# Kernel optimization log

Measured on AMD Instinct MI355X. Metric: run time of the kernel, lower is better.

The kernel has to match this reference:

```python
import jax, jax.numpy as jnp
import numpy as np

D_MODEL = 1024
N_HEADS = 16
D_K = D_MODEL // N_HEADS
NEG_INF = -1e30


def setup_inputs() -> dict:
    key = jax.random.key(0)
    ks = jax.random.split(key, 12)
    B, S = 4, 2048
    scale = 1.0 / np.sqrt(D_MODEL)
    inp = {
        "query": jax.random.normal(ks[0], (B, S, D_MODEL), jnp.float32),
        "key": jax.random.normal(ks[1], (B, S, D_MODEL), jnp.float32),
        "value": jax.random.normal(ks[2], (B, S, D_MODEL), jnp.float32),
        "mask": jax.random.randint(ks[3], (B, S, S), 0, 2, jnp.int32),
        "w_q": jax.random.normal(ks[4], (D_MODEL, D_MODEL), jnp.float32) * scale,
        "b_q": jnp.zeros((D_MODEL,), jnp.float32),
        "w_k": jax.random.normal(ks[5], (D_MODEL, D_MODEL), jnp.float32) * scale,
        "b_k": jnp.zeros((D_MODEL,), jnp.float32),
        "w_v": jax.random.normal(ks[6], (D_MODEL, D_MODEL), jnp.float32) * scale,
        "b_v": jnp.zeros((D_MODEL,), jnp.float32),
        "w_o": jax.random.normal(ks[7], (D_MODEL, D_MODEL), jnp.float32) * scale,
        "b_o": jnp.zeros((D_MODEL,), jnp.float32),
    }
    return inp


def reference(query, key, value, mask, w_q, b_q, w_k, b_k, w_v, b_v, w_o, b_o):
    B, Sq, _ = query.shape
    Sk = key.shape[1]
    # Linear projections (torch nn.Linear: x @ W.T + b), split into heads
    Q = (query @ w_q.T + b_q).reshape(B, Sq, N_HEADS, D_K).transpose(0, 2, 1, 3)
    K = (key @ w_k.T + b_k).reshape(B, Sk, N_HEADS, D_K).transpose(0, 2, 1, 3)
    V = (value @ w_v.T + b_v).reshape(B, Sk, N_HEADS, D_K).transpose(0, 2, 1, 3)
    # scores: (B, H, Sq, Sk)
    scores = jnp.einsum('bhqd,bhkd->bhqk', Q, K) / jnp.sqrt(jnp.float32(D_K))
    scores = jnp.where(mask[:, None, :, :] == 0, NEG_INF, scores)
    attn = jax.nn.softmax(scores, axis=-1)  # dropout p=0 -> identity (eval)
    context = jnp.einsum('bhqk,bhkd->bhqd', attn, V)
    context = context.transpose(0, 2, 1, 3).reshape(B, Sq, D_MODEL)
    return context @ w_o.T + b_o
```

## Files before the change

### kernel.cpp

```cpp
#include <hip/hip_runtime.h>
#include <hip/hip_bf16.h>
#include <stdint.h>

#define DM 1024
#define NHEADS 16
#define DK 64
#define BB 4
#define SS 2048

typedef unsigned short u16;
typedef __bf16 bf16x8 __attribute__((ext_vector_type(8)));
typedef __bf16 bf16x4 __attribute__((ext_vector_type(4)));
typedef float f32x4 __attribute__((ext_vector_type(4)));

#if __has_builtin(__builtin_amdgcn_exp2f)
#define EXP2(x) __builtin_amdgcn_exp2f(x)
#else
#define EXP2(x) exp2f(x)
#endif

static __device__ __forceinline__ u16 f2bf(float f) {
    union { float f; uint32_t u; } v; v.f = f;
    uint32_t r = v.u + 0x7fffu + ((v.u >> 16) & 1u);
    return (u16)(r >> 16);
}

static __device__ __forceinline__ f32x4 mfma16(bf16x8 a, bf16x8 b, f32x4 c) {
    return __builtin_amdgcn_mfma_f32_16x16x32_bf16(a, b, c, 0, 0, 0);
}

static __device__ __forceinline__ void gload16(const u16* g, u16* l) {
    __builtin_amdgcn_global_load_lds((const __attribute__((address_space(1))) void*)g,
                                     (__attribute__((address_space(3))) void*)l, 16, 0, 0);
}

#define PREP_W 4096
#define PREP_X 12288
#define PREP_M 2048
__global__ __launch_bounds__(256) void k_prep(const float* __restrict__ wq, const float* __restrict__ wk,
                                              const float* __restrict__ wv, const float* __restrict__ wo,
                                              u16* __restrict__ wout,
                                              const float* __restrict__ xq, const float* __restrict__ xk,
                                              const float* __restrict__ xv, u16* __restrict__ xout,
                                              const int* __restrict__ mask, uint32_t* __restrict__ bits) {
    const int bid = blockIdx.x, tid = threadIdx.x;
    if (bid < PREP_W) {
        int t = bid * 256 + tid;
        int which = t >> 18;
        int off = (t & 0x3FFFF) << 2;
        const float* src = (which == 0) ? wq : (which == 1) ? wk : (which == 2) ? wv : wo;
        float4 v = *(const float4*)(src + off);
        ushort4 o;
        o.x = f2bf(v.x); o.y = f2bf(v.y); o.z = f2bf(v.z); o.w = f2bf(v.w);
        *(ushort4*)(wout + ((size_t)which << 20) + off) = o;
    } else if (bid < PREP_W + PREP_X) {
        int lb = bid - PREP_W;
        int which = lb >> 12;
        const float* src = (which == 0) ? xq : (which == 1) ? xk : xv;
        size_t base = (((size_t)(lb & 4095)) * 256 + tid) * 8;
        float4 v0 = *(const float4*)(src + base);
        float4 v1 = *(const float4*)(src + base + 4);
        union { u16 s[8]; uint4 u; } p;
        p.s[0]=f2bf(v0.x); p.s[1]=f2bf(v0.y); p.s[2]=f2bf(v0.z); p.s[3]=f2bf(v0.w);
        p.s[4]=f2bf(v1.x); p.s[5]=f2bf(v1.y); p.s[6]=f2bf(v1.z); p.s[7]=f2bf(v1.w);
        *(uint4*)(xout + ((size_t)which << 23) + base) = p.u;
    } else {
        int lb = bid - PREP_W - PREP_X;
        int gid = lb * 256 + tid;
        int lane = gid & 63;
        int wv_ = gid >> 6;
        const int nw = (PREP_M * 256) >> 6;
        const long totalInts = (long)BB * SS * SS;
        for (long base = (long)wv_ * 64; base < totalInts; base += (long)nw * 64) {
            int m = mask[base + lane];
            unsigned long long bal = __ballot(m != 0);
            if (lane == 0)  bits[(base >> 5)]     = (uint32_t)bal;
            if (lane == 32) bits[(base >> 5) + 1] = (uint32_t)(bal >> 32);
        }
    }
}

template<int MODE>
__global__ __launch_bounds__(256) void k_proj(const u16* __restrict__ X, const u16* __restrict__ W,
                                              const float* __restrict__ bias, void* __restrict__ Yv,
                                              float alpha) {
    __shared__ u16 Ab[128 * 32];
    __shared__ u16 Bb[128 * 32];
    const int tid = threadIdx.x;
    const int lane = tid & 63, wv = tid >> 6;
    const int wr = wv >> 1, wc = wv & 1;
    const int lrow = lane & 15, lgrp = lane >> 4;
    const int m0 = (blockIdx.x >> 3) * 128;
    const int n0 = (blockIdx.x & 7) * 128;
    const int trow = tid >> 2;
    const int tk = (tid & 3) * 8;

    f32x4 acc[4][4] = {};

    for (int kk = 0; kk < DM; kk += 32) {
#pragma unroll
        for (int i = 0; i < 2; ++i) {
            gload16(X + (size_t)(m0 + i * 64 + trow) * DM + kk + tk, &Ab[(i * 256 + tid) * 8]);
            gload16(W + (size_t)(n0 + i * 64 + trow) * DM + kk + tk, &Bb[(i * 256 + tid) * 8]);
        }
        __syncthreads();
        bf16x8 af[4], bfr[4];
#pragma unroll
        for (int i = 0; i < 4; ++i)
            af[i] = *(const bf16x8*)&Ab[(wr * 64 + i * 16 + lrow) * 32 + lgrp * 8];
#pragma unroll
        for (int j = 0; j < 4; ++j)
            bfr[j] = *(const bf16x8*)&Bb[(wc * 64 + j * 16 + lrow) * 32 + lgrp * 8];
#pragma unroll
        for (int i = 0; i < 4; ++i)
#pragma unroll
            for (int j = 0; j < 4; ++j)
                acc[i][j] = mfma16(af[i], bfr[j], acc[i][j]);
        __syncthreads();
    }

#pragma unroll
    for (int j = 0; j < 4; ++j) {
        int n = n0 + wc * 64 + j * 16 + lrow;
        float bv = bias[n];
        int h = n >> 6, d = n & 63;
#pragma unroll
        for (int i = 0; i < 4; ++i) {
            int mbase = m0 + wr * 64 + i * 16 + (lgrp << 2);
            if (MODE == 0) {
                u16* Y = (u16*)Yv;
#pragma unroll
                for (int r = 0; r < 4; ++r) {
                    int m = mbase + r;
                    int b = m >> 11, s = m & 2047;
                    Y[(((size_t)(b * NHEADS + h) * SS) + s) * DK + d] = f2bf((acc[i][j][r] + bv) * alpha);
                }
            } else if (MODE == 1) {
                int b = mbase >> 11, s = mbase & 2047;
                ushort4 o;
                o.x = f2bf(acc[i][j][0] + bv);
                o.y = f2bf(acc[i][j][1] + bv);
                o.z = f2bf(acc[i][j][2] + bv);
                o.w = f2bf(acc[i][j][3] + bv);
                *(ushort4*)&((u16*)Yv)[(((size_t)(b * NHEADS + h) * DK) + d) * SS + s] = o;
            } else {
                float* Y = (float*)Yv;
#pragma unroll
                for (int r = 0; r < 4; ++r)
                    Y[(size_t)(mbase + r) * DM + n] = acc[i][j][r] + bv;
            }
        }
    }
}

#define NT (SS / 64)
__global__ __launch_bounds__(512, 4) void k_attn(const u16* __restrict__ Q, const u16* __restrict__ K,
                                                 const u16* __restrict__ VT, const uint32_t* __restrict__ mbits,
                                                 u16* __restrict__ ctx) {
    __shared__ u16 Kt[2][64 * 64];
    __shared__ u16 Vt[2][64 * 64];
    __shared__ u16 Pl[8][2][16][72];
    const int tid = threadIdx.x;
    const int lane = tid & 63, w = tid >> 6;
    const int lrow = lane & 15, lgrp = lane >> 4;
    const int bid = blockIdx.x;
    const int bh = bid & 63;
    const int qt = bid >> 6;
    const int b = bh >> 4, h = bh & 15;
    const int qbase = qt * 256 + w * 32;

    const u16* Qh = Q + (size_t)bh * SS * DK;
    const u16* Kh = K + (size_t)bh * SS * DK;
    const u16* Vh = VT + (size_t)bh * DK * SS;

    bf16x8 qf[2][2];
#pragma unroll
    for (int s = 0; s < 2; ++s) {
        const u16* p = Qh + (size_t)(qbase + 16 * s + lrow) * DK + lgrp * 8;
        qf[s][0] = *(const bf16x8*)(p);
        qf[s][1] = *(const bf16x8*)(p + 32);
    }

    const uint64_t* mrow[2];
#pragma unroll
    for (int s = 0; s < 2; ++s)
        mrow[s] = (const uint64_t*)mbits + ((size_t)(b * SS + qbase + 16 * s + lrow)) * (SS / 64);

    union { uint4 u; bf16x8 v; } onesu;
    onesu.u = make_uint4(0x3F803F80u, 0x3F803F80u, 0x3F803F80u, 0x3F803F80u);
    const bf16x8 ones = onesu.v;

    const int swzA = (lgrp * 8) ^ ((lrow & 7) * 8);
    const int swzB = (32 + lgrp * 8) ^ ((lrow & 7) * 8);

    const int srow = tid >> 3;
    const int ssrc = ((tid & 7) * 8) ^ ((srow & 7) * 8);

    f32x4 acc[2][4] = {};
    f32x4 asum[2] = {};

    gload16(Kh + (size_t)srow * DK + ssrc, &Kt[0][tid * 8]);
    gload16(Vh + (size_t)srow * SS + ssrc, &Vt[0][tid * 8]);
    __syncthreads();

    int cur = 0;
    for (int kt = 0; kt < NT; ++kt) {
        if (kt + 1 < NT) {
            gload16(Kh + (size_t)((kt + 1) * 64 + srow) * DK + ssrc, &Kt[cur ^ 1][tid * 8]);
            gload16(Vh + (size_t)srow * SS + (kt + 1) * 64 + ssrc, &Vt[cur ^ 1][tid * 8]);
        }
        uint64_t wm2[2];
#pragma unroll
        for (int s = 0; s < 2; ++s) wm2[s] = mrow[s][kt];

        const u16* Kc = Kt[cur];
        const u16* Vc = Vt[cur];
        bf16x8 pf[2][2];
#pragma unroll
        for (int s = 0; s < 2; ++s) {
            f32x4 st[4] = {};
#pragma unroll
            for (int t = 0; t < 4; ++t) {
                bf16x8 ka = *(const bf16x8*)&Kc[(16 * t + lrow) * 64 + swzA];
                bf16x8 kb = *(const bf16x8*)&Kc[(16 * t + lrow) * 64 + swzB];
                st[t] = mfma16(ka, qf[s][0], st[t]);
                st[t] = mfma16(kb, qf[s][1], st[t]);
            }
            const uint64_t wm = wm2[s];
#pragma unroll
            for (int t = 0; t < 4; ++t) {
                uint32_t wt = (uint32_t)(wm >> (16 * t + 4 * lgrp));
                bf16x4 pk;
#pragma unroll
                for (int r = 0; r < 4; ++r) {
                    float p = EXP2(st[t][r]);
                    p = ((wt >> r) & 1u) ? p : 0.0f;
                    pk[r] = (__bf16)p;
                }
                *(bf16x4*)&Pl[w][s][lrow][16 * t + 4 * lgrp] = pk;
            }
            pf[s][0] = *(const bf16x8*)&Pl[w][s][lrow][lgrp * 8];
            pf[s][1] = *(const bf16x8*)&Pl[w][s][lrow][32 + lgrp * 8];
            asum[s] = mfma16(pf[s][0], ones, asum[s]);
            asum[s] = mfma16(pf[s][1], ones, asum[s]);
        }
#pragma unroll
        for (int dt = 0; dt < 4; ++dt) {
            bf16x8 vf0 = *(const bf16x8*)&Vc[(16 * dt + lrow) * 64 + swzA];
            bf16x8 vf1 = *(const bf16x8*)&Vc[(16 * dt + lrow) * 64 + swzB];
#pragma unroll
            for (int s = 0; s < 2; ++s) {
                acc[s][dt] = mfma16(pf[s][0], vf0, acc[s][dt]);
                acc[s][dt] = mfma16(pf[s][1], vf1, acc[s][dt]);
            }
        }
        __syncthreads();
        cur ^= 1;
    }

#pragma unroll
    for (int s = 0; s < 2; ++s)
#pragma unroll
        for (int r = 0; r < 4; ++r) {
            float li = 1.0f / asum[s][r];
            int q = qbase + 16 * s + 4 * lgrp + r;
#pragma unroll
            for (int dt = 0; dt < 4; ++dt)
                ctx[((size_t)b * SS + q) * DM + h * 64 + dt * 16 + lrow] = f2bf(acc[s][dt][r] * li);
        }
}

extern "C" void kernel_launch(void* const* d_in, const int* in_sizes, int n_in,
                              void* d_out, int out_size, void* d_ws, size_t ws_size,
                              hipStream_t stream) {
    const float* query = (const float*)d_in[0];
    const float* key   = (const float*)d_in[1];
    const float* value = (const float*)d_in[2];
    const int*   mask  = (const int*)d_in[3];
    const float* w_q   = (const float*)d_in[4];
    const float* b_q   = (const float*)d_in[5];
    const float* w_k   = (const float*)d_in[6];
    const float* b_k   = (const float*)d_in[7];
    const float* w_v   = (const float*)d_in[8];
    const float* b_v   = (const float*)d_in[9];
    const float* w_o   = (const float*)d_in[10];
    const float* b_o   = (const float*)d_in[11];
    float* out = (float*)d_out;

    char* ws = (char*)d_ws;
    u16*      Wb = (u16*)(ws);
    uint32_t* mb = (uint32_t*)(ws + (8u  << 20));
    u16*      Xq = (u16*)(ws + (16u << 20));
    u16*      Xk = (u16*)(ws + (32u << 20));
    u16*      Xv = (u16*)(ws + (48u << 20));
    u16*      Qw = (u16*)(ws + (64u << 20));
    u16*      Kw = (u16*)(ws + (80u << 20));
    u16*      Vw = (u16*)(ws + (96u << 20));
    u16*      Cw = (u16*)(ws + (112u << 20));

    const float qscale = 0.125f * 1.4426950408889634f;

    k_prep<<<dim3(PREP_W + PREP_X + PREP_M), dim3(256), 0, stream>>>(
        w_q, w_k, w_v, w_o, Wb, query, key, value, Xq, mask, mb);
    k_proj<0><<<dim3(512), dim3(256), 0, stream>>>(Xq, Wb,              b_q, Qw, qscale);
    k_proj<0><<<dim3(512), dim3(256), 0, stream>>>(Xk, Wb + (1u << 20), b_k, Kw, 1.0f);
    k_proj<1><<<dim3(512), dim3(256), 0, stream>>>(Xv, Wb + (2u << 20), b_v, Vw, 1.0f);
    k_attn<<<dim3(512), dim3(512), 0, stream>>>(Qw, Kw, Vw, mb, Cw);
    k_proj<2><<<dim3(512), dim3(256), 0, stream>>>(Cw, Wb + (3u << 20), b_o, out, 1.0f);
}
```

Baseline: 278.7 us.

## Merge QKV projections into one launch and shrink attention P buffer

Combines the three Q/K/V projection GEMM launches into a single 1536-block kernel that selects inputs by block index, reducing launch overhead and tail effects. The attention kernel reuses one LDS P-staging slot per wave instead of two, halving that buffer, and raises the launch-bounds occupancy hint from 4 to 6. The tighter register budget may cause spills in the attention kernel.

```diff
diff --git a/kernel.cpp b/kernel.cpp
--- a/kernel.cpp
+++ b/kernel.cpp
@@ -80,10 +80,85 @@
     }
 }
 
-template<int MODE>
-__global__ __launch_bounds__(256) void k_proj(const u16* __restrict__ X, const u16* __restrict__ W,
-                                              const float* __restrict__ bias, void* __restrict__ Yv,
-                                              float alpha) {
+__global__ __launch_bounds__(256) void k_projqkv(const u16* __restrict__ Xq, const u16* __restrict__ Xk,
+                                                 const u16* __restrict__ Xv, const u16* __restrict__ Wb,
+                                                 const float* __restrict__ bq, const float* __restrict__ bk,
+                                                 const float* __restrict__ bv,
+                                                 u16* __restrict__ Qw, u16* __restrict__ Kw,
+                                                 u16* __restrict__ Vw, float qscale) {
+    __shared__ u16 Ab[128 * 32];
+    __shared__ u16 Bb[128 * 32];
+    const int sel = blockIdx.x >> 9;
+    const int tile = blockIdx.x & 511;
+    const u16* X = (sel == 0) ? Xq : (sel == 1) ? Xk : Xv;
+    const u16* W = Wb + ((size_t)sel << 20);
+    const float* bias = (sel == 0) ? bq : (sel == 1) ? bk : bv;
+    u16* Y = (sel == 0) ? Qw : (sel == 1) ? Kw : Vw;
+    const float alpha = (sel == 0) ? qscale : 1.0f;
+
+    const int tid = threadIdx.x;
+    const int lane = tid & 63, wv = tid >> 6;
+    const int wr = wv >> 1, wc = wv & 1;
+    const int lrow = lane & 15, lgrp = lane >> 4;
+    const int m0 = (tile >> 3) * 128;
+    const int n0 = (tile & 7) * 128;
+    const int trow = tid >> 2;
+    const int tk = (tid & 3) * 8;
+
+    f32x4 acc[4][4] = {};
+
+    for (int kk = 0; kk < DM; kk += 32) {
+#pragma unroll
+        for (int i = 0; i < 2; ++i) {
+            gload16(X + (size_t)(m0 + i * 64 + trow) * DM + kk + tk, &Ab[(i * 256 + tid) * 8]);
+            gload16(W + (size_t)(n0 + i * 64 + trow) * DM + kk + tk, &Bb[(i * 256 + tid) * 8]);
+        }
+        __syncthreads();
+        bf16x8 af[4], bfr[4];
+#pragma unroll
+        for (int i = 0; i < 4; ++i)
+            af[i] = *(const bf16x8*)&Ab[(wr * 64 + i * 16 + lrow) * 32 + lgrp * 8];
+#pragma unroll
+        for (int j = 0; j < 4; ++j)
+            bfr[j] = *(const bf16x8*)&Bb[(wc * 64 + j * 16 + lrow) * 32 + lgrp * 8];
+#pragma unroll
+        for (int i = 0; i < 4; ++i)
+#pragma unroll
+            for (int j = 0; j < 4; ++j)
+                acc[i][j] = mfma16(af[i], bfr[j], acc[i][j]);
+        __syncthreads();
+    }
+
+#pragma unroll
+    for (int j = 0; j < 4; ++j) {
+        int n = n0 + wc * 64 + j * 16 + lrow;
+        float bv_ = bias[n];
+        int h = n >> 6, d = n & 63;
+#pragma unroll
+        for (int i = 0; i < 4; ++i) {
+            int mbase = m0 + wr * 64 + i * 16 + (lgrp << 2);
+            if (sel != 2) {
+#pragma unroll
+                for (int r = 0; r < 4; ++r) {
+                    int m = mbase + r;
+                    int b = m >> 11, s = m & 2047;
+                    Y[(((size_t)(b * NHEADS + h) * SS) + s) * DK + d] = f2bf((acc[i][j][r] + bv_) * alpha);
+                }
+            } else {
+                int b = mbase >> 11, s = mbase & 2047;
+                ushort4 o;
+                o.x = f2bf(acc[i][j][0] + bv_);
+                o.y = f2bf(acc[i][j][1] + bv_);
+                o.z = f2bf(acc[i][j][2] + bv_);
+                o.w = f2bf(acc[i][j][3] + bv_);
+                *(ushort4*)&Y[(((size_t)(b * NHEADS + h) * DK) + d) * SS + s] = o;
+            }
+        }
+    }
+}
+
+__global__ __launch_bounds__(256) void k_oproj(const u16* __restrict__ X, const u16* __restrict__ W,
+                                               const float* __restrict__ bias, float* __restrict__ out) {
     __shared__ u16 Ab[128 * 32];
     __shared__ u16 Bb[128 * 32];
     const int tid = threadIdx.x;
@@ -123,43 +198,23 @@
     for (int j = 0; j < 4; ++j) {
         int n = n0 + wc * 64 + j * 16 + lrow;
         float bv = bias[n];
-        int h = n >> 6, d = n & 63;
 #pragma unroll
         for (int i = 0; i < 4; ++i) {
             int mbase = m0 + wr * 64 + i * 16 + (lgrp << 2);
-            if (MODE == 0) {
-                u16* Y = (u16*)Yv;
-#pragma unroll
-                for (int r = 0; r < 4; ++r) {
-                    int m = mbase + r;
-                    int b = m >> 11, s = m & 2047;
-                    Y[(((size_t)(b * NHEADS + h) * SS) + s) * DK + d] = f2bf((acc[i][j][r] + bv) * alpha);
-                }
-            } else if (MODE == 1) {
-                int b = mbase >> 11, s = mbase & 2047;
-                ushort4 o;
-                o.x = f2bf(acc[i][j][0] + bv);
-                o.y = f2bf(acc[i][j][1] + bv);
-                o.z = f2bf(acc[i][j][2] + bv);
-                o.w = f2bf(acc[i][j][3] + bv);
-                *(ushort4*)&((u16*)Yv)[(((size_t)(b * NHEADS + h) * DK) + d) * SS + s] = o;
-            } else {
-                float* Y = (float*)Yv;
-#pragma unroll
-                for (int r = 0; r < 4; ++r)
-                    Y[(size_t)(mbase + r) * DM + n] = acc[i][j][r] + bv;
-            }
+#pragma unroll
+            for (int r = 0; r < 4; ++r)
+                out[(size_t)(mbase + r) * DM + n] = acc[i][j][r] + bv;
         }
     }
 }
 
 #define NT (SS / 64)
-__global__ __launch_bounds__(512, 4) void k_attn(const u16* __restrict__ Q, const u16* __restrict__ K,
+__global__ __launch_bounds__(512, 6) void k_attn(const u16* __restrict__ Q, const u16* __restrict__ K,
                                                  const u16* __restrict__ VT, const uint32_t* __restrict__ mbits,
                                                  u16* __restrict__ ctx) {
     __shared__ u16 Kt[2][64 * 64];
     __shared__ u16 Vt[2][64 * 64];
-    __shared__ u16 Pl[8][2][16][72];
+    __shared__ u16 Pl[8][16][72];
     const int tid = threadIdx.x;
     const int lane = tid & 63, w = tid >> 6;
     const int lrow = lane & 15, lgrp = lane >> 4;
@@ -237,10 +292,10 @@
                     p = ((wt >> r) & 1u) ? p : 0.0f;
                     pk[r] = (__bf16)p;
                 }
-                *(bf16x4*)&Pl[w][s][lrow][16 * t + 4 * lgrp] = pk;
+                *(bf16x4*)&Pl[w][lrow][16 * t + 4 * lgrp] = pk;
             }
-            pf[s][0] = *(const bf16x8*)&Pl[w][s][lrow][lgrp * 8];
-            pf[s][1] = *(const bf16x8*)&Pl[w][s][lrow][32 + lgrp * 8];
+            pf[s][0] = *(const bf16x8*)&Pl[w][lrow][lgrp * 8];
+            pf[s][1] = *(const bf16x8*)&Pl[w][lrow][32 + lgrp * 8];
             asum[s] = mfma16(pf[s][0], ones, asum[s]);
             asum[s] = mfma16(pf[s][1], ones, asum[s]);
         }
@@ -302,9 +357,8 @@
 
     k_prep<<<dim3(PREP_W + PREP_X + PREP_M), dim3(256), 0, stream>>>(
         w_q, w_k, w_v, w_o, Wb, query, key, value, Xq, mask, mb);
-    k_proj<0><<<dim3(512), dim3(256), 0, stream>>>(Xq, Wb,              b_q, Qw, qscale);
-    k_proj<0><<<dim3(512), dim3(256), 0, stream>>>(Xk, Wb + (1u << 20), b_k, Kw, 1.0f);
-    k_proj<1><<<dim3(512), dim3(256), 0, stream>>>(Xv, Wb + (2u << 20), b_v, Vw, 1.0f);
+    k_projqkv<<<dim3(1536), dim3(256), 0, stream>>>(Xq, Xk, Xv, Wb, b_q, b_k, b_v,
+                                                    Qw, Kw, Vw, qscale);
     k_attn<<<dim3(512), dim3(512), 0, stream>>>(Qw, Kw, Vw, mb, Cw);
-    k_proj<2><<<dim3(512), dim3(256), 0, stream>>>(Cw, Wb + (3u << 20), b_o, out, 1.0f);
-}
+    k_oproj<<<dim3(512), dim3(256), 0, stream>>>(Cw, Wb + (3u << 20), b_o, out);
+}
```

After: 612.5 us. +119.8%, slower.
